# Performance work log

Measured on AMD Instinct MI355X. Metric: run time of the kernel, lower is better.

The kernel has to match this reference:

```python
import jax, jax.numpy as jnp
import numpy as np

N = 100000   # ntoken / num nodes
D = 256      # ninp
E = 3200000  # num edges
BN_EPS = 1e-5


def gcn_conv(x, W, b, src, dst, num_nodes):
    """PyG GCNConv: add self-loops, symmetric deg normalization, aggregate at dst."""
    loop = jnp.arange(num_nodes, dtype=src.dtype)
    src = jnp.concatenate([src, loop])
    dst = jnp.concatenate([dst, loop])
    deg = jax.ops.segment_sum(jnp.ones_like(dst, dtype=x.dtype), dst,
                              num_segments=num_nodes)
    dinv = jnp.where(deg > 0, jax.lax.rsqrt(deg), 0.0)
    norm = dinv[src] * dinv[dst]          # [E+N]
    xw = x @ W                            # [N, out]
    msg = xw[src] * norm[:, None]         # gather + scale
    out = jax.ops.segment_sum(msg, dst, num_segments=num_nodes)
    return out + b


def batch_norm(x, gamma, beta):
    # training-mode BatchNorm1d over node dim (biased variance)
    mean = jnp.mean(x, axis=0)
    var = jnp.mean((x - mean) ** 2, axis=0)
    return gamma * (x - mean) * jax.lax.rsqrt(var + BN_EPS) + beta


def setup_inputs() -> dict:
    key = jax.random.key(0)
    ks = jax.random.split(key, 5)
    edge_index = jax.random.randint(ks[0], (2, E), 0, N, dtype=jnp.int64)
    emb_weight = jax.random.normal(ks[1], (N, D), dtype=jnp.float32) * 0.05
    W1 = jax.random.normal(ks[2], (D, 2 * D), dtype=jnp.float32) * 0.05
    b1 = jnp.zeros((2 * D,), dtype=jnp.float32)
    W2 = jax.random.normal(ks[3], (2 * D, D), dtype=jnp.float32) * 0.05
    b2 = jnp.zeros((D,), dtype=jnp.float32)
    gamma = jnp.ones((D,), dtype=jnp.float32)
    beta = jnp.zeros((D,), dtype=jnp.float32)
    return {"edge_index": edge_index, "emb_weight": emb_weight,
            "W1": W1, "b1": b1, "W2": W2, "b2": b2,
            "gamma": gamma, "beta": beta}


def reference(edge_index, emb_weight, W1, b1, W2, b2, gamma, beta):
    src, dst = edge_index[0], edge_index[1]
    h = gcn_conv(emb_weight, W1, b1, src, dst, N)   # [N, 2D]
    # dropout is identity in eval / deterministic reference
    h = gcn_conv(h, W2, b2, src, dst, N)            # [N, D]
    return batch_norm(h, gamma, beta)
```

## Files before the change

### kernel.cpp

```cpp
#include <hip/hip_runtime.h>
#include <hip/hip_fp16.h>
#include <math.h>

#define DIM   256
#define DIM4  64
#define DIMH2 64
#define BN_EPS 1e-5f

typedef __attribute__((ext_vector_type(8))) _Float16 half8;
typedef __attribute__((ext_vector_type(4))) float f32x4;

__device__ __forceinline__ unsigned h2u(__half2 h) { return __builtin_bit_cast(unsigned, h); }
__device__ __forceinline__ __half2 u2h(unsigned u) { return __builtin_bit_cast(__half2, u); }

__global__ void k_deg_init(int* __restrict__ deg, int N) {
    int i = blockIdx.x * blockDim.x + threadIdx.x;
    if (i < N) deg[i] = 1;
}

__global__ void k_deg_count(const int* __restrict__ dst, int* __restrict__ deg, int E) {
    for (int e = blockIdx.x * blockDim.x + threadIdx.x; e < E; e += gridDim.x * blockDim.x) {
        atomicAdd(&deg[dst[e]], 1);
    }
}

__global__ void k_dinv(const int* __restrict__ deg, float* __restrict__ dinv, int N) {
    int i = blockIdx.x * blockDim.x + threadIdx.x;
    if (i < N) dinv[i] = rsqrtf((float)deg[i]);
}

__global__ __launch_bounds__(256) void k_tohalf(const float4* __restrict__ in,
                                                uint2* __restrict__ outh, int n4) {
    for (int i = blockIdx.x * blockDim.x + threadIdx.x; i < n4; i += gridDim.x * blockDim.x) {
        float4 v = in[i];
        uint2 o;
        o.x = h2u(__halves2half2(__float2half_rn(v.x), __float2half_rn(v.y)));
        o.y = h2u(__halves2half2(__float2half_rn(v.z), __float2half_rn(v.w)));
        outh[i] = o;
    }
}

__global__ void k_scan_partial(const int* __restrict__ deg, int* __restrict__ part, int N) {
    __shared__ int sh[256];
    int base = blockIdx.x * 1024 + threadIdx.x * 4;
    int s = 0;
#pragma unroll
    for (int q = 0; q < 4; ++q) {
        int i = base + q;
        if (i < N) s += deg[i] - 1;
    }
    sh[threadIdx.x] = s;
    __syncthreads();
    for (int off = 128; off > 0; off >>= 1) {
        if (threadIdx.x < off) sh[threadIdx.x] += sh[threadIdx.x + off];
        __syncthreads();
    }
    if (threadIdx.x == 0) part[blockIdx.x] = sh[0];
}

__global__ void k_scan_offsets(int* __restrict__ part, int* __restrict__ rowstart, int nb, int N) {
    int run = 0;
    for (int i = 0; i < nb; ++i) { int v = part[i]; part[i] = run; run += v; }
    rowstart[N] = run;
}

__global__ void k_scan_write(const int* __restrict__ deg, const int* __restrict__ part,
                             int* __restrict__ rowstart, int* __restrict__ cursor, int N) {
    __shared__ int sh[256];
    int base = blockIdx.x * 1024 + threadIdx.x * 4;
    int v[4]; int s = 0;
#pragma unroll
    for (int q = 0; q < 4; ++q) {
        int i = base + q;
        v[q] = (i < N) ? deg[i] - 1 : 0;
        s += v[q];
    }
    sh[threadIdx.x] = s;
    __syncthreads();
    if (threadIdx.x == 0) {
        int run = part[blockIdx.x];
        for (int t = 0; t < 256; ++t) { int x = sh[t]; sh[t] = run; run += x; }
    }
    __syncthreads();
    int run = sh[threadIdx.x];
#pragma unroll
    for (int q = 0; q < 4; ++q) {
        int i = base + q;
        if (i < N) { rowstart[i] = run; cursor[i] = run; run += v[q]; }
    }
}

__global__ void k_fill(const int* __restrict__ src, const int* __restrict__ dst,
                       int* __restrict__ cursor, int* __restrict__ col, int E) {
    for (int e = blockIdx.x * blockDim.x + threadIdx.x; e < E; e += gridDim.x * blockDim.x) {
        int d = dst[e];
        int p = atomicAdd(&cursor[d], 1);
        col[p] = src[e];
    }
}

__global__ __launch_bounds__(256) void k_agg_h2h(const uint2* __restrict__ xh,
                                                 const float* __restrict__ dinv,
                                                 const int* __restrict__ rowstart,
                                                 const int* __restrict__ col,
                                                 uint2* __restrict__ outh,
                                                 float* __restrict__ rs, int N, int writeRs) {
    int wave = (blockIdx.x * blockDim.x + threadIdx.x) >> 6;
    int lane = threadIdx.x & 63;
    if (wave >= N) return;
    float di = dinv[wave];
    uint2 xraw = xh[(size_t)wave * DIMH2 + lane];
    float2 f0 = __half22float2(u2h(xraw.x));
    float2 f1 = __half22float2(u2h(xraw.y));
    float ax = di * f0.x, ay = di * f0.y, az = di * f1.x, aw = di * f1.y;
    float sd = 0.f;
    int p = rowstart[wave], e = rowstart[wave + 1];
    if (p < e) {
        int j = col[p]; float dj = dinv[j];
        for (++p; p < e; ++p) {
            int jn = col[p]; float djn = dinv[jn];
            uint2 raw = xh[(size_t)j * DIMH2 + lane];
            float2 v0 = __half22float2(u2h(raw.x));
            float2 v1 = __half22float2(u2h(raw.y));
            ax += dj * v0.x; ay += dj * v0.y; az += dj * v1.x; aw += dj * v1.y;
            sd += dj;
            j = jn; dj = djn;
        }
        uint2 raw = xh[(size_t)j * DIMH2 + lane];
        float2 v0 = __half22float2(u2h(raw.x));
        float2 v1 = __half22float2(u2h(raw.y));
        ax += dj * v0.x; ay += dj * v0.y; az += dj * v1.x; aw += dj * v1.y;
        sd += dj;
    }
    uint2 o;
    o.x = h2u(__halves2half2(__float2half_rn(di * ax), __float2half_rn(di * ay)));
    o.y = h2u(__halves2half2(__float2half_rn(di * az), __float2half_rn(di * aw)));
    outh[(size_t)wave * DIMH2 + lane] = o;
    if (writeRs && lane == 0) rs[wave] = di * (sd + di);
}

__global__ void k_wct(const float* __restrict__ W1, const float* __restrict__ W2,
                      _Float16* __restrict__ WcT) {
    int i = blockIdx.x, j = threadIdx.x;
    float acc = 0.f;
    for (int k = 0; k < 2 * DIM; ++k) acc += W1[i * 2 * DIM + k] * W2[k * DIM + j];
    WcT[(size_t)j * DIM + i] = (_Float16)acc;
}

__global__ void k_cvec(const float* __restrict__ b1, const float* __restrict__ W2,
                       float* __restrict__ cvec) {
    int j = threadIdx.x;
    float acc = 0.f;
    for (int k = 0; k < 2 * DIM; ++k) acc += b1[k] * W2[k * DIM + j];
    cvec[j] = acc;
}

#define GBM 128
#define GBN 128
#define ASTR 40

__global__ __launch_bounds__(256) void k_gemm_mfma(const _Float16* __restrict__ Ah,
                                                   const _Float16* __restrict__ BTh,
                                                   const float* __restrict__ rs,
                                                   const float* __restrict__ cvec,
                                                   const float* __restrict__ b2,
                                                   float* __restrict__ C, int N) {
    __shared__ _Float16 As[GBM][ASTR];
    __shared__ _Float16 Bs[GBN][ASTR];
    int tid  = threadIdx.x;
    int row0 = blockIdx.x * GBM;
    int col0 = blockIdx.y * GBN;
    int w    = tid >> 6;
    int lane = tid & 63;
    int wr   = (w >> 1) * 64;
    int wc   = (w & 1) * 64;
    int lr   = lane & 15;
    int kg   = lane >> 4;

    f32x4 acc[4][4];
#pragma unroll
    for (int i = 0; i < 4; ++i)
#pragma unroll
        for (int j = 0; j < 4; ++j) acc[i][j] = (f32x4)0.f;

    int sr = tid >> 2;
    int sc = (tid & 3) * 8;

    for (int k0 = 0; k0 < DIM; k0 += 32) {
        __syncthreads();
#pragma unroll
        for (int q = 0; q < 2; ++q) {
            int r  = sr + q * 64;
            int gr = row0 + r;
            half8 av = (half8)(_Float16)0.f;
            if (gr < N)
                av = *reinterpret_cast<const half8*>(&Ah[(size_t)gr * DIM + k0 + sc]);
            *reinterpret_cast<half8*>(&As[r][sc]) = av;
            half8 bv = *reinterpret_cast<const half8*>(&BTh[(size_t)(col0 + r) * DIM + k0 + sc]);
            *reinterpret_cast<half8*>(&Bs[r][sc]) = bv;
        }
        __syncthreads();

        half8 af[4], bf[4];
#pragma unroll
        for (int mm = 0; mm < 4; ++mm)
            af[mm] = *reinterpret_cast<const half8*>(&As[wr + mm * 16 + lr][kg * 8]);
#pragma unroll
        for (int nn = 0; nn < 4; ++nn)
            bf[nn] = *reinterpret_cast<const half8*>(&Bs[wc + nn * 16 + lr][kg * 8]);
#pragma unroll
        for (int mm = 0; mm < 4; ++mm)
#pragma unroll
            for (int nn = 0; nn < 4; ++nn)
                acc[mm][nn] = __builtin_amdgcn_mfma_f32_16x16x32_f16(af[mm], bf[nn],
                                                                     acc[mm][nn], 0, 0, 0);
    }

#pragma unroll
    for (int mm = 0; mm < 4; ++mm) {
        int rbase = row0 + wr + mm * 16 + kg * 4;
#pragma unroll
        for (int reg = 0; reg < 4; ++reg) {
            int r = rbase + reg;
            if (r < N) {
                float rv = rs[r];
#pragma unroll
                for (int nn = 0; nn < 4; ++nn) {
                    int c = col0 + wc + nn * 16 + lr;
                    C[(size_t)r * DIM + c] = acc[mm][nn][reg] + rv * cvec[c] + b2[c];
                }
            }
        }
    }
}

__global__ void k_bnzero(float* __restrict__ p) {
    p[threadIdx.x] = 0.f;
}

__global__ __launch_bounds__(256) void k_bnstats(const float* __restrict__ h,
                                                 float* __restrict__ sum,
                                                 float* __restrict__ sq, int N) {
    int ch = threadIdx.x;
    float s = 0.f, ss = 0.f;
    for (int r = blockIdx.x; r < N; r += gridDim.x) {
        float v = h[r * DIM + ch];
        s += v; ss += v * v;
    }
    atomicAdd(&sum[ch], s);
    atomicAdd(&sq[ch], ss);
}

__global__ void k_bnfinal(const float* __restrict__ sum, const float* __restrict__ sq,
                          const float* __restrict__ gamma, const float* __restrict__ beta,
                          float* __restrict__ scale, float* __restrict__ shift, int N) {
    int ch = threadIdx.x;
    float invN = 1.0f / (float)N;
    float mean = sum[ch] * invN;
    float var = sq[ch] * invN - mean * mean;
    float inv = rsqrtf(var + BN_EPS);
    float sc = gamma[ch] * inv;
    scale[ch] = sc;
    shift[ch] = beta[ch] - mean * sc;
}

__global__ __launch_bounds__(256) void k_bnnorm(float4* __restrict__ out,
                                                const float4* __restrict__ scale,
                                                const float4* __restrict__ shift, int n4) {
    for (int i = blockIdx.x * blockDim.x + threadIdx.x; i < n4; i += gridDim.x * blockDim.x) {
        int j = i & (DIM4 - 1);
        float4 v = out[i];
        float4 sc = scale[j];
        float4 sh = shift[j];
        v.x = v.x * sc.x + sh.x;
        v.y = v.y * sc.y + sh.y;
        v.z = v.z * sc.z + sh.z;
        v.w = v.w * sc.w + sh.w;
        out[i] = v;
    }
}

extern "C" void kernel_launch(void* const* d_in, const int* in_sizes, int n_in,
                              void* d_out, int out_size, void* d_ws, size_t ws_size,
                              hipStream_t stream) {
    const int* ei        = (const int*)d_in[0];
    const float* emb     = (const float*)d_in[1];
    const float* W1      = (const float*)d_in[2];
    const float* b1      = (const float*)d_in[3];
    const float* W2      = (const float*)d_in[4];
    const float* b2      = (const float*)d_in[5];
    const float* gamma   = (const float*)d_in[6];
    const float* beta    = (const float*)d_in[7];

    const int E = in_sizes[0] / 2;
    const int N = in_sizes[1] / DIM;
    const int* src = ei;
    const int* dst = ei + E;

    char* w = (char*)d_ws;
    size_t off = 0;
    auto alloc = [&](size_t bytes) -> void* {
        off = (off + 255) & ~(size_t)255;
        void* p = w + off;
        off += bytes;
        return p;
    };
    int*      deg      = (int*)     alloc((size_t)N * 4);
    float*    dinv     = (float*)   alloc((size_t)N * 4);
    int*      rowstart = (int*)     alloc((size_t)(N + 1) * 4);
    int*      cursor   = (int*)     alloc((size_t)N * 4);
    int*      part     = (int*)     alloc(1024);
    int*      csr_col  = (int*)     alloc((size_t)E * 4);
    float*    rs       = (float*)   alloc((size_t)N * 4);
    uint2*    agg2h    = (uint2*)   alloc((size_t)N * DIM * 2);
    _Float16* WcTh     = (_Float16*)alloc((size_t)DIM * DIM * 2);
    float*    cvec     = (float*)   alloc(DIM * 4);
    float*    bnsum    = (float*)   alloc(2 * DIM * 4);
    float*    bnscale  = (float*)   alloc(2 * DIM * 4);

    uint2* xh    = (uint2*)d_out;
    uint2* agg1h = (uint2*)((char*)d_out + (size_t)N * DIM * 2);
    float* out   = (float*)d_out;

    const int nb1024 = (N + 1023) / 1024;

    k_deg_init<<<(N + 255) / 256, 256, 0, stream>>>(deg, N);
    k_deg_count<<<2048, 256, 0, stream>>>(dst, deg, E);
    k_dinv<<<(N + 255) / 256, 256, 0, stream>>>(deg, dinv, N);

    k_tohalf<<<2048, 256, 0, stream>>>((const float4*)emb, xh, N * DIM4);

    k_scan_partial<<<nb1024, 256, 0, stream>>>(deg, part, N);
    k_scan_offsets<<<1, 1, 0, stream>>>(part, rowstart, nb1024, N);
    k_scan_write<<<nb1024, 256, 0, stream>>>(deg, part, rowstart, cursor, N);
    k_fill<<<2048, 256, 0, stream>>>(src, dst, cursor, csr_col, E);

    k_agg_h2h<<<(N + 3) / 4, 256, 0, stream>>>(xh, dinv, rowstart, csr_col, agg1h, rs, N, 1);
    k_agg_h2h<<<(N + 3) / 4, 256, 0, stream>>>(agg1h, dinv, rowstart, csr_col, agg2h, rs, N, 0);

    k_wct<<<DIM, DIM, 0, stream>>>(W1, W2, WcTh);
    k_cvec<<<1, DIM, 0, stream>>>(b1, W2, cvec);

    dim3 ggrid((N + GBM - 1) / GBM, DIM / GBN);
    k_gemm_mfma<<<ggrid, 256, 0, stream>>>((const _Float16*)agg2h, WcTh, rs, cvec, b2, out, N);

    k_bnzero<<<1, 512, 0, stream>>>(bnsum);
    k_bnstats<<<512, 256, 0, stream>>>(out, bnsum, bnsum + DIM, N);
    k_bnfinal<<<1, DIM, 0, stream>>>(bnsum, bnsum + DIM, gamma, beta,
                                     bnscale, bnscale + DIM, N);
    k_bnnorm<<<2048, 256, 0, stream>>>((float4*)out, (const float4*)bnscale,
                                       (const float4*)(bnscale + DIM), N * DIM4);
}
```

Before: 1.281 ms.

## Build CSR via two-level bucketed binning instead of per-edge global atomics

Replaces the per-edge global atomicAdd CSR fill with a two-pass scheme. The first pass bins edges into 256-node buckets using shared-memory histograms and one global atomic per bucket per block, staging (src,dst) pairs. The second pass scatters each bucket into shared memory to order it, then writes columns out coalesced. This aims to remove contended, scattered global atomics and random writes, at the cost of an extra E*8-byte staging buffer and one more pass over the edges.

```diff
diff --git a/kernel.cpp b/kernel.cpp
--- a/kernel.cpp
+++ b/kernel.cpp
@@ -6,6 +6,10 @@
 #define DIM4  64
 #define DIMH2 64
 #define BN_EPS 1e-5f
+
+#define NPB      256
+#define MAXBUCK  512
+#define CAP      13312
 
 typedef __attribute__((ext_vector_type(8))) _Float16 half8;
 typedef __attribute__((ext_vector_type(4))) float f32x4;
@@ -65,7 +69,7 @@
 }
 
 __global__ void k_scan_write(const int* __restrict__ deg, const int* __restrict__ part,
-                             int* __restrict__ rowstart, int* __restrict__ cursor, int N) {
+                             int* __restrict__ rowstart, int N) {
     __shared__ int sh[256];
     int base = blockIdx.x * 1024 + threadIdx.x * 4;
     int v[4]; int s = 0;
@@ -86,16 +90,77 @@
 #pragma unroll
     for (int q = 0; q < 4; ++q) {
         int i = base + q;
-        if (i < N) { rowstart[i] = run; cursor[i] = run; run += v[q]; }
-    }
-}
-
-__global__ void k_fill(const int* __restrict__ src, const int* __restrict__ dst,
-                       int* __restrict__ cursor, int* __restrict__ col, int E) {
-    for (int e = blockIdx.x * blockDim.x + threadIdx.x; e < E; e += gridDim.x * blockDim.x) {
+        if (i < N) { rowstart[i] = run; run += v[q]; }
+    }
+}
+
+__global__ void k_bucket_init(const int* __restrict__ rowstart, int* __restrict__ gcur,
+                              int N, int nbuck) {
+    int b = blockIdx.x * blockDim.x + threadIdx.x;
+    if (b < nbuck) {
+        int n = b * NPB;
+        gcur[b] = rowstart[n < N ? n : N];
+    }
+}
+
+__global__ __launch_bounds__(256) void k_binfill(const int* __restrict__ src,
+                                                 const int* __restrict__ dst,
+                                                 int* __restrict__ gcur,
+                                                 uint2* __restrict__ stage,
+                                                 int E, int nbuck) {
+    __shared__ int hist[MAXBUCK];
+    __shared__ int base[MAXBUCK];
+    int tid = threadIdx.x;
+    int chunk = (E + gridDim.x - 1) / gridDim.x;
+    int e0 = blockIdx.x * chunk;
+    int e1 = min(E, e0 + chunk);
+    for (int b = tid; b < nbuck; b += 256) hist[b] = 0;
+    __syncthreads();
+    for (int e = e0 + tid; e < e1; e += 256)
+        atomicAdd(&hist[dst[e] >> 8], 1);
+    __syncthreads();
+    for (int b = tid; b < nbuck; b += 256)
+        base[b] = atomicAdd(&gcur[b], hist[b]);
+    __syncthreads();
+    for (int b = tid; b < nbuck; b += 256) hist[b] = 0;
+    __syncthreads();
+    for (int e = e0 + tid; e < e1; e += 256) {
         int d = dst[e];
-        int p = atomicAdd(&cursor[d], 1);
-        col[p] = src[e];
+        int bk = d >> 8;
+        int p = base[bk] + atomicAdd(&hist[bk], 1);
+        stage[p] = make_uint2((unsigned)src[e], (unsigned)d);
+    }
+}
+
+__global__ __launch_bounds__(256) void k_csrbuild(const uint2* __restrict__ stage,
+                                                  const int* __restrict__ rowstart,
+                                                  int* __restrict__ col, int N) {
+    __shared__ int cur[NPB];
+    __shared__ int lcol[CAP];
+    int b   = blockIdx.x;
+    int tid = threadIdx.x;
+    int n0  = b << 8;
+    int n1  = min(N, n0 + NPB);
+    int r0  = rowstart[n0];
+    int r1  = rowstart[n1];
+    int cnt = r1 - r0;
+    if (n0 + tid < n1) cur[tid] = rowstart[n0 + tid] - r0;
+    __syncthreads();
+    if (cnt <= CAP) {
+        for (int i = tid; i < cnt; i += 256) {
+            uint2 rec = stage[r0 + i];
+            int p = atomicAdd(&cur[(int)rec.y - n0], 1);
+            lcol[p] = (int)rec.x;
+        }
+        __syncthreads();
+        for (int i = tid; i < cnt; i += 256)
+            col[r0 + i] = lcol[i];
+    } else {
+        for (int i = tid; i < cnt; i += 256) {
+            uint2 rec = stage[r0 + i];
+            int p = atomicAdd(&cur[(int)rec.y - n0], 1);
+            col[r0 + p] = (int)rec.x;
+        }
     }
 }
 
@@ -296,6 +361,7 @@
     const int N = in_sizes[1] / DIM;
     const int* src = ei;
     const int* dst = ei + E;
+    const int nbuck = (N + NPB - 1) / NPB;
 
     char* w = (char*)d_ws;
     size_t off = 0;
@@ -308,9 +374,10 @@
     int*      deg      = (int*)     alloc((size_t)N * 4);
     float*    dinv     = (float*)   alloc((size_t)N * 4);
     int*      rowstart = (int*)     alloc((size_t)(N + 1) * 4);
-    int*      cursor   = (int*)     alloc((size_t)N * 4);
+    int*      gcur     = (int*)     alloc((size_t)(nbuck + 1) * 4);
     int*      part     = (int*)     alloc(1024);
     int*      csr_col  = (int*)     alloc((size_t)E * 4);
+    uint2*    stage    = (uint2*)   alloc((size_t)E * 8);
     float*    rs       = (float*)   alloc((size_t)N * 4);
     uint2*    agg2h    = (uint2*)   alloc((size_t)N * DIM * 2);
     _Float16* WcTh     = (_Float16*)alloc((size_t)DIM * DIM * 2);
@@ -332,8 +399,10 @@
 
     k_scan_partial<<<nb1024, 256, 0, stream>>>(deg, part, N);
     k_scan_offsets<<<1, 1, 0, stream>>>(part, rowstart, nb1024, N);
-    k_scan_write<<<nb1024, 256, 0, stream>>>(deg, part, rowstart, cursor, N);
-    k_fill<<<2048, 256, 0, stream>>>(src, dst, cursor, csr_col, E);
+    k_scan_write<<<nb1024, 256, 0, stream>>>(deg, part, rowstart, N);
+    k_bucket_init<<<(nbuck + 255) / 256, 256, 0, stream>>>(rowstart, gcur, N, nbuck);
+    k_binfill<<<256, 256, 0, stream>>>(src, dst, gcur, stage, E, nbuck);
+    k_csrbuild<<<nbuck, 256, 0, stream>>>(stage, rowstart, csr_col, N);
 
     k_agg_h2h<<<(N + 3) / 4, 256, 0, stream>>>(xh, dinv, rowstart, csr_col, agg1h, rs, N, 1);
     k_agg_h2h<<<(N + 3) / 4, 256, 0, stream>>>(agg1h, dinv, rowstart, csr_col, agg2h, rs, N, 0);
```

After: 1.091 ms. 14.8% less time.
